# Performance work log

Measured on AMD Instinct MI355X. Metric: run time of the kernel, lower is better.

The kernel has to match this reference:

```python
import jax, jax.numpy as jnp
import numpy as np

N_NODES = 100000
N_EDGES = 1000000
NUM_GRAPHS = 100
EPS_BN = 1e-5
EPS_GATE = 1e-6


def _bn(x, gamma, beta):
    # BatchNorm1d in training mode: batch statistics over dim 0
    mu = jnp.mean(x, axis=0)
    var = jnp.var(x, axis=0)
    return (x - mu) * jax.lax.rsqrt(var + EPS_BN) * gamma + beta


def _gated_gcn_layer(h, e, snorm_n, snorm_e, W, b, g_h, b_h, g_e, b_e, src, dst):
    # W: [5, d, d] stacking A, B, C, D, E projections; b: [5, d]
    Ah = h @ W[0] + b[0]
    Bh = h @ W[1] + b[1]
    Ce = e @ W[2] + b[2]
    Dh = h @ W[3] + b[3]
    Eh = h @ W[4] + b[4]
    # edge update: e_ji = Dh_src + Eh_dst + Ce   [E, d]
    e_new = Dh[src] + Eh[dst] + Ce
    sigma = jax.nn.sigmoid(e_new)
    # node update: gated sum of source messages at destination nodes
    num = jax.ops.segment_sum(sigma * Bh[src], dst, num_segments=h.shape[0])
    den = jax.ops.segment_sum(sigma, dst, num_segments=h.shape[0])
    h_new = Ah + num / (den + EPS_GATE)
    # graph size normalization
    h_new = h_new * snorm_n
    e_new = e_new * snorm_e
    # batch norm + relu + residual (dropout = 0.0)
    h_new = jax.nn.relu(_bn(h_new, g_h, b_h))
    e_new = jax.nn.relu(_bn(e_new, g_e, b_e))
    return h + h_new, e + e_new


def setup_inputs() -> dict:
    key = jax.random.key(0)
    ks = jax.random.split(key, 12)
    nodes_feat = jax.random.normal(ks[0], (N_NODES, 64), jnp.float32)
    edges_feat = jax.random.normal(ks[1], (N_EDGES, 1), jnp.float32)
    snorm_n = jax.random.uniform(ks[2], (N_NODES, 1), jnp.float32)
    snorm_e = jax.random.uniform(ks[3], (N_EDGES, 1), jnp.float32)
    src = jax.random.randint(ks[4], (N_EDGES,), 0, N_NODES, jnp.int32)
    dst = jax.random.randint(ks[5], (N_EDGES,), 0, N_NODES, jnp.int32)
    node_graph_ids = jnp.sort(jax.random.randint(ks[6], (N_NODES,), 0, NUM_GRAPHS, jnp.int32))
    Wh = jax.random.normal(ks[7], (64, 70), jnp.float32) * 0.1
    bh = jnp.zeros((70,), jnp.float32)
    We = jax.random.normal(ks[8], (1, 70), jnp.float32) * 0.1
    be = jnp.zeros((70,), jnp.float32)
    W_gcn = jax.random.normal(ks[9], (3, 5, 70, 70), jnp.float32) * 0.1
    b_gcn = jnp.zeros((3, 5, 70), jnp.float32)
    bn_gamma_h = jnp.ones((3, 70), jnp.float32)
    bn_beta_h = jnp.zeros((3, 70), jnp.float32)
    bn_gamma_e = jnp.ones((3, 70), jnp.float32)
    bn_beta_e = jnp.zeros((3, 70), jnp.float32)
    return {"nodes_feat": nodes_feat, "edges_feat": edges_feat, "snorm_n": snorm_n,
            "snorm_e": snorm_e, "src": src, "dst": dst, "node_graph_ids": node_graph_ids,
            "Wh": Wh, "bh": bh, "We": We, "be": be, "W_gcn": W_gcn, "b_gcn": b_gcn,
            "bn_gamma_h": bn_gamma_h, "bn_beta_h": bn_beta_h,
            "bn_gamma_e": bn_gamma_e, "bn_beta_e": bn_beta_e}


def reference(nodes_feat, edges_feat, snorm_n, snorm_e, src, dst, node_graph_ids,
              Wh, bh, We, be, W_gcn, b_gcn, bn_gamma_h, bn_beta_h, bn_gamma_e, bn_beta_e):
    h = nodes_feat @ Wh + bh
    e = edges_feat @ We + be
    # hidden_dims = [70, 70] -> only gated_gcn_1 (params index 0) and gated_gcn_o (index 2)
    for li in (0, 2):
        h, e = _gated_gcn_layer(h, e, snorm_n, snorm_e, W_gcn[li], b_gcn[li],
                                bn_gamma_h[li], bn_beta_h[li], bn_gamma_e[li], bn_beta_e[li],
                                src, dst)
    # dgl.mean_nodes: per-graph mean of node features
    sums = jax.ops.segment_sum(h, node_graph_ids, num_segments=NUM_GRAPHS)
    counts = jax.ops.segment_sum(jnp.ones((h.shape[0],), h.dtype), node_graph_ids,
                                 num_segments=NUM_GRAPHS)
    hg = sums / jnp.maximum(counts, 1.0)[:, None]
    return hg
```

## Files before the change

### kernel.cpp

```cpp
#include <hip/hip_runtime.h>

#define NN 100000
#define NE 1000000
#define NG 100
#define DD 70
#define EL0 64
#define CH0 (9 * EL0)
#define TPW 5
#define EPW (16 * TPW)
#define EPB (10 * EPW)
#define SCB 512
#define WTS (70 * 72)

typedef __attribute__((ext_vector_type(8))) short bf16x8;
typedef __attribute__((ext_vector_type(4))) float f32x4;

__device__ __forceinline__ float sigmoidf_(float x) { return 1.f / (1.f + expf(-x)); }

__device__ __forceinline__ unsigned int rne_bf16(float x) {
    unsigned int u = __float_as_uint(x);
    return (u + 0x7FFFu + ((u >> 16) & 1u)) >> 16;
}
__device__ __forceinline__ float b2f(unsigned short u) {
    return __uint_as_float(((unsigned int)u) << 16);
}

#define DOT4(acc, vv, ww) { acc = fmaf((vv).x, (ww).x, acc); acc = fmaf((vv).y, (ww).y, acc); \
                            acc = fmaf((vv).z, (ww).z, acc); acc = fmaf((vv).w, (ww).w, acc); }

__global__ void k_trAll(const float* __restrict__ Wh, const float* __restrict__ Wg,
                        float* __restrict__ WT) {
    int m = blockIdx.y, f = blockIdx.x, k = threadIdx.x;
    const float* W;
    int K = DD;
    switch (m) {
        case 0: W = Wh; K = 64; break;
        case 1: W = Wg + 0 * 4900; break;
        case 2: W = Wg + 1 * 4900; break;
        case 3: W = Wg + 3 * 4900; break;
        case 4: W = Wg + 4 * 4900; break;
        case 5: W = Wg + 10 * 4900; break;
        case 6: W = Wg + 11 * 4900; break;
        case 7: W = Wg + 13 * 4900; break;
        default: W = Wg + 14 * 4900; break;
    }
    if (k < 72) WT[(m * 70 + f) * 72 + k] = (k < K) ? W[k * DD + f] : 0.f;
}

#define DENSE_BODY(STORE)                                                         \
    __shared__ float sx[36 * 72];                                                 \
    int t = threadIdx.x;                                                          \
    int r = t / DD, f = t - r * DD;                                               \
    long rb = (long)blockIdx.x * 36;                                              \
    for (int idx = t; idx < 36 * 72; idx += 640) {                                \
        int rr = idx / 72, kk = idx - rr * 72;                                    \
        long i = rb + rr;                                                         \
        sx[idx] = (kk < K && i < nrows) ? x[i * K + kk] : 0.f;                    \
    }                                                                             \
    __syncthreads();                                                              \
    if (r < 9) {                                                                  \
        const float4* wr = (const float4*)(WTm + f * 72);                         \
        float bb = bias[f];                                                       \
        float a0 = bb, a1 = bb, a2 = bb, a3 = bb;                                 \
        const float4* s0 = (const float4*)&sx[(r) * 72];                          \
        const float4* s1 = (const float4*)&sx[(r + 9) * 72];                      \
        const float4* s2 = (const float4*)&sx[(r + 18) * 72];                     \
        const float4* s3 = (const float4*)&sx[(r + 27) * 72];                     \
        _Pragma("unroll 1")                                                       \
        for (int q = 0; q < 18; q += 2) {                                         \
            float4 wA = wr[q], wB = wr[q + 1];                                    \
            float4 vA0 = s0[q], vB0 = s0[q + 1];                                  \
            DOT4(a0, vA0, wA) DOT4(a0, vB0, wB)                                   \
            float4 vA1 = s1[q], vB1 = s1[q + 1];                                  \
            DOT4(a1, vA1, wA) DOT4(a1, vB1, wB)                                   \
            float4 vA2 = s2[q], vB2 = s2[q + 1];                                  \
            DOT4(a2, vA2, wA) DOT4(a2, vB2, wB)                                   \
            float4 vA3 = s3[q], vB3 = s3[q + 1];                                  \
            DOT4(a3, vA3, wA) DOT4(a3, vB3, wB)                                   \
        }                                                                         \
        long i0 = rb + r, i1 = i0 + 9, i2 = i0 + 18, i3 = i0 + 27;                \
        if (i0 < nrows) STORE(i0, a0);                                            \
        if (i1 < nrows) STORE(i1, a1);                                            \
        if (i2 < nrows) STORE(i2, a2);                                            \
        if (i3 < nrows) STORE(i3, a3);                                            \
    }

__global__ __launch_bounds__(640) void k_dense_r(const float* __restrict__ x, int K,
                                                 const float* __restrict__ WTm,
                                                 const float* __restrict__ bias,
                                                 float* __restrict__ out, int nrows) {
#define ST_F32(ii, aa) out[(ii) * DD + f] = (aa)
    DENSE_BODY(ST_F32)
#undef ST_F32
}

__global__ __launch_bounds__(640) void k_dense_rh(const float* __restrict__ x, int K,
                                                  const float* __restrict__ WTm,
                                                  const float* __restrict__ bias,
                                                  unsigned short* __restrict__ out, int nrows) {
#define ST_BF16(ii, aa) out[(ii) * DD + f] = (unsigned short)rne_bf16(aa)
    DENSE_BODY(ST_BF16)
#undef ST_BF16
}

__global__ void k_pre(const float* __restrict__ We, const float* __restrict__ be,
                      const float* __restrict__ Wg, const float* __restrict__ bg,
                      float* __restrict__ v1, float* __restrict__ v2) {
    int f = threadIdx.x;
    if (f < DD) {
        const float* W2 = Wg + 2 * DD * DD;
        const float* b2 = bg + 2 * DD;
        float a = 0.f, c = 0.f;
        for (int k = 0; k < DD; ++k) {
            a = fmaf(We[k], W2[k * DD + f], a);
            c = fmaf(be[k], W2[k * DD + f], c);
        }
        v1[f] = a;
        v2[f] = c + b2[f];
    }
}

__global__ void k_prep2(const float* __restrict__ v1, const float* __restrict__ v2,
                        const float* __restrict__ murs_e, const float* __restrict__ ge,
                        const float* __restrict__ bbe, const float* __restrict__ We,
                        const float* __restrict__ be, const float* __restrict__ Wg,
                        float* __restrict__ CT2, unsigned short* __restrict__ WB) {
    int t = threadIdx.x;
    if (t < 35) {
        int f0 = 2 * t, f1 = 2 * t + 1;
        float A0 = murs_e[DD + f0] * ge[f0], A1 = murs_e[DD + f1] * ge[f1];
        float* c = CT2 + t * 12;
        c[0] = v1[f0];  c[1] = v1[f1];
        c[2] = v2[f0];  c[3] = v2[f1];
        c[4] = A0;      c[5] = A1;
        c[6] = bbe[f0] - murs_e[f0] * A0;
        c[7] = bbe[f1] - murs_e[f1] * A1;
        c[8] = We[f0];  c[9] = We[f1];
        c[10] = be[f0]; c[11] = be[f1];
    }
    const float* WC2 = Wg + 12 * 4900;
    for (int idx = t; idx < 960; idx += 512) {
        int nt = idx / 192, rem = idx - nt * 192;
        int c = rem / 64, l = rem - c * 64;
        int n = nt * 16 + (l & 15);
        int kb = c * 32 + (l >> 4) * 8;
        for (int j = 0; j < 8; ++j) {
            int k = kb + j;
            unsigned short v = 0;
            if (k < 70 && n < 70) v = (unsigned short)rne_bf16(WC2[k * 70 + n]);
            WB[((nt * 3 + c) * 64 + l) * 8 + j] = v;
        }
    }
}

__global__ void k_count(const int* __restrict__ dst, int* __restrict__ off) {
    int j = blockIdx.x * 256 + threadIdx.x;
    if (j < NE) atomicAdd(&off[dst[j]], 1);
}

__global__ void k_scan_a(int* __restrict__ off, int* __restrict__ part) {
    __shared__ int s[SCB];
    int t = threadIdx.x, i = blockIdx.x * SCB + t;
    int v = (i < NN) ? off[i] : 0;
    s[t] = v;
    __syncthreads();
    for (int d = 1; d < SCB; d <<= 1) {
        int x = (t >= d) ? s[t - d] : 0;
        __syncthreads();
        s[t] += x;
        __syncthreads();
    }
    if (i < NN) off[i] = s[t] - v;
    if (t == SCB - 1) part[blockIdx.x] = s[t];
}

__global__ void k_scan_b(int* __restrict__ part, int nb) {
    __shared__ int s[256];
    int t = threadIdx.x;
    int v = (t < nb) ? part[t] : 0;
    s[t] = v;
    __syncthreads();
    for (int d = 1; d < 256; d <<= 1) {
        int x = (t >= d) ? s[t - d] : 0;
        __syncthreads();
        s[t] += x;
        __syncthreads();
    }
    if (t < nb) part[t] = s[t] - v;
}

__global__ void k_scan_c(int* __restrict__ off, const int* __restrict__ part) {
    int i = blockIdx.x * SCB + threadIdx.x;
    if (i < NN) off[i] += part[blockIdx.x];
}

__global__ void k_fill(const int* __restrict__ src, const int* __restrict__ dst,
                       const float* __restrict__ ef, const float* __restrict__ sne,
                       int* __restrict__ off, int* __restrict__ src_s,
                       float* __restrict__ ef_s, float* __restrict__ sne_s,
                       int* __restrict__ dst_s) {
    int j = blockIdx.x * 256 + threadIdx.x;
    if (j < NE) {
        int d = dst[j];
        int pos = atomicAdd(&off[d], 1);
        src_s[pos] = src[j];
        ef_s[pos] = ef[j];
        sne_s[pos] = sne[j];
        dst_s[pos] = d;
    }
}

__global__ __launch_bounds__(640) void k_edge0(
    const float* __restrict__ ef_s, const float* __restrict__ sne_s,
    const int* __restrict__ src_s, const int* __restrict__ dst_s,
    const unsigned short* __restrict__ PB, const unsigned short* __restrict__ PD,
    const unsigned short* __restrict__ PE, const float* __restrict__ v1,
    const float* __restrict__ v2, float* __restrict__ num,
    float* __restrict__ den, float* __restrict__ red) {
    int t = threadIdx.x;
    int r = t / DD, f = t - r * DD;
    bool act = (r < 9);
    float c1 = 0.f, c2 = 0.f;
    if (act) { c1 = v1[f]; c2 = v2[f]; }
    float acc_s = 0.f, acc_q = 0.f;
    int e_beg = blockIdx.x * CH0 + r * EL0;
    bool live = act && e_beg < NE;
    int dcur = 0;
    float accn = 0.f, accd = 0.f;
    int lim = 0;
    if (live) {
        dcur = dst_s[e_beg];
        lim = NE - e_beg;
        if (lim > EL0) lim = EL0;
    }
    for (int g = 0; g < lim; g += 4) {
        int m = lim - g;
        if (m > 4) m = 4;
        int dj[4];
        float pdj[4], pbj[4], pej[4], efj[4], snj[4];
#pragma unroll
        for (int j = 0; j < 4; ++j) {
            if (j < m) {
                int e = e_beg + g + j;
                int s = src_s[e];
                int d = dst_s[e];
                dj[j] = d;
                efj[j] = ef_s[e];
                snj[j] = sne_s[e];
                pdj[j] = b2f(PD[(long)s * DD + f]);
                pbj[j] = b2f(PB[(long)s * DD + f]);
                pej[j] = b2f(PE[(long)d * DD + f]);
            }
        }
#pragma unroll
        for (int j = 0; j < 4; ++j) {
            if (j < m) {
                if (dj[j] != dcur) {
                    unsafeAtomicAdd(&num[(long)dcur * DD + f], accn);
                    unsafeAtomicAdd(&den[(long)dcur * DD + f], accd);
                    accn = 0.f; accd = 0.f;
                    dcur = dj[j];
                }
                float en = pdj[j] + pej[j] + efj[j] * c1 + c2;
                float sg = sigmoidf_(en);
                accn = fmaf(sg, pbj[j], accn);
                accd += sg;
                float tv = en * snj[j];
                acc_s += tv;
                acc_q = fmaf(tv, tv, acc_q);
            }
        }
    }
    if (live) {
        unsafeAtomicAdd(&num[(long)dcur * DD + f], accn);
        unsafeAtomicAdd(&den[(long)dcur * DD + f], accd);
    }
    __shared__ float ss[DD], sq[DD];
    if (t < DD) { ss[t] = 0.f; sq[t] = 0.f; }
    __syncthreads();
    if (act) { atomicAdd(&ss[f], acc_s); atomicAdd(&sq[f], acc_q); }
    __syncthreads();
    if (t < DD) {
        atomicAdd(&red[t], ss[t]);
        atomicAdd(&red[DD + t], sq[t]);
    }
}

__global__ __launch_bounds__(640) void k_edge2(
    const float* __restrict__ ef_s, const float* __restrict__ sne_s,
    const int* __restrict__ src_s, const int* __restrict__ dst_s,
    const unsigned short* __restrict__ PD0, const unsigned short* __restrict__ PE0,
    const unsigned short* __restrict__ PB2, const unsigned short* __restrict__ PD2,
    const unsigned short* __restrict__ PE2, const float* __restrict__ CT2,
    const unsigned short* __restrict__ WB, const float* __restrict__ bC2,
    float* __restrict__ num, float* __restrict__ den) {
    __shared__ __align__(16) unsigned short As[10 * 16 * 104];
    int t = threadIdx.x;
    int w = t >> 6, l = t & 63;
    unsigned short* Aw = &As[w * 1664];
    for (int i = l; i < 832; i += 64) ((unsigned int*)Aw)[i] = 0u;
    int wb_e = blockIdx.x * EPB + w * EPW;
    if (wb_e >= NE) return;
    int col = l & 15, hi = l >> 4;
    bf16x8 bfr[15];
#pragma unroll
    for (int q = 0; q < 15; ++q)
        bfr[q] = *(const bf16x8*)(WB + (q * 64 + l) * 8);
    float bc[5];
#pragma unroll
    for (int nt = 0; nt < 5; ++nt) bc[nt] = bC2[nt * 16 + col];
    int e0p = wb_e + hi * 4;
    if (e0p > NE - 1) e0p = NE - 1;
    int dcur = dst_s[e0p];
    float an[5], ad[5];
#pragma unroll
    for (int nt = 0; nt < 5; ++nt) { an[nt] = 0.f; ad[nt] = 0.f; }
    for (int tt = 0; tt < TPW; ++tt) {
        int et = wb_e + tt * 16;
        if (et >= NE) break;
        for (int i = l; i < 560; i += 64) {
            int el = i / 35, fp = i - el * 35, f = fp * 2;
            int e = et + el;
            unsigned int val = 0u;
            if (e < NE) {
                int s = src_s[e], d = dst_s[e];
                float efv = ef_s[e], sn = sne_s[e];
                const float* ct = CT2 + fp * 12;
                unsigned int upd = *(const unsigned int*)(PD0 + (long)s * DD + f);
                unsigned int upe = *(const unsigned int*)(PE0 + (long)d * DD + f);
                float pdx = __uint_as_float(upd << 16);
                float pdy = __uint_as_float(upd & 0xFFFF0000u);
                float pex = __uint_as_float(upe << 16);
                float pey = __uint_as_float(upe & 0xFFFF0000u);
                float en0a = pdx + pex + efv * ct[0] + ct[2];
                float en0b = pdy + pey + efv * ct[1] + ct[3];
                float ra = fmaxf(fmaf(en0a * sn, ct[4], ct[6]), 0.f);
                float rb = fmaxf(fmaf(en0b * sn, ct[5], ct[7]), 0.f);
                float e1a = fmaf(efv, ct[8], ct[10]) + ra;
                float e1b = fmaf(efv, ct[9], ct[11]) + rb;
                val = rne_bf16(e1a) | (rne_bf16(e1b) << 16);
            }
            ((unsigned int*)Aw)[(el * 104 + f) >> 1] = val;
        }
        bf16x8 af[3];
#pragma unroll
        for (int c = 0; c < 3; ++c)
            af[c] = *(const bf16x8*)(Aw + (l & 15) * 104 + c * 32 + hi * 8);
        f32x4 acc[5];
#pragma unroll
        for (int nt = 0; nt < 5; ++nt) {
            acc[nt] = (f32x4){0.f, 0.f, 0.f, 0.f};
#pragma unroll
            for (int c = 0; c < 3; ++c)
                acc[nt] = __builtin_amdgcn_mfma_f32_16x16x32_bf16(af[c], bfr[nt * 3 + c],
                                                                  acc[nt], 0, 0, 0);
        }
#pragma unroll
        for (int j = 0; j < 4; ++j) {
            int e = et + hi * 4 + j;
            if (e < NE) {
                int d = dst_s[e];
                if (d != dcur) {
#pragma unroll
                    for (int nt = 0; nt < 5; ++nt) {
                        int nv = nt * 16 + col;
                        if (nv < 70) {
                            unsafeAtomicAdd(&num[(long)dcur * DD + nv], an[nt]);
                            unsafeAtomicAdd(&den[(long)dcur * DD + nv], ad[nt]);
                        }
                        an[nt] = 0.f; ad[nt] = 0.f;
                    }
                    dcur = d;
                }
                int s = src_s[e];
#pragma unroll
                for (int nt = 0; nt < 5; ++nt) {
                    int nv = nt * 16 + col;
                    if (nv < 70) {
                        float en = acc[nt][j] + bc[nt] + b2f(PD2[(long)s * DD + nv])
                                 + b2f(PE2[(long)d * DD + nv]);
                        float sg = sigmoidf_(en);
                        an[nt] = fmaf(sg, b2f(PB2[(long)s * DD + nv]), an[nt]);
                        ad[nt] += sg;
                    }
                }
            }
        }
    }
#pragma unroll
    for (int nt = 0; nt < 5; ++nt) {
        int nv = nt * 16 + col;
        if (nv < 70) {
            unsafeAtomicAdd(&num[(long)dcur * DD + nv], an[nt]);
            unsafeAtomicAdd(&den[(long)dcur * DD + nv], ad[nt]);
        }
    }
}

__global__ __launch_bounds__(640) void k_nstats(const float* __restrict__ PA,
                                                const float* __restrict__ num,
                                                const float* __restrict__ den,
                                                const float* __restrict__ snn,
                                                float* __restrict__ red) {
    int t = threadIdx.x;
    int r = t / DD, f = t - r * DD;
    bool act = (r < 9);
    float acc_s = 0.f, acc_q = 0.f;
    const int T = (NN + 8) / 9;
    for (int tile = blockIdx.x; tile < T; tile += gridDim.x) {
        int i = tile * 9 + r;
        if (act && i < NN) {
            long o = (long)i * DD + f;
            float v = (PA[o] + num[o] / (den[o] + 1e-6f)) * snn[i];
            acc_s += v;
            acc_q = fmaf(v, v, acc_q);
        }
    }
    __shared__ float ss[DD], sq[DD];
    if (t < DD) { ss[t] = 0.f; sq[t] = 0.f; }
    __syncthreads();
    if (act) { atomicAdd(&ss[f], acc_s); atomicAdd(&sq[f], acc_q); }
    __syncthreads();
    if (t < DD) {
        atomicAdd(&red[t], ss[t]);
        atomicAdd(&red[DD + t], sq[t]);
    }
}

__global__ void k_stats(const float* __restrict__ sums, float* __restrict__ murs, float invn) {
    int f = threadIdx.x;
    if (f < DD) {
        float mu = sums[f] * invn;
        float var = sums[DD + f] * invn - mu * mu;
        murs[f] = mu;
        murs[DD + f] = rsqrtf(var + 1e-5f);
    }
}

__global__ __launch_bounds__(256) void k_apply(const float* __restrict__ hin,
                                               const float* __restrict__ PA,
                                               const float* __restrict__ num,
                                               const float* __restrict__ den,
                                               const float* __restrict__ snn,
                                               const float* __restrict__ murs,
                                               const float* __restrict__ g,
                                               const float* __restrict__ b,
                                               float* __restrict__ hout) {
    long idx = (long)blockIdx.x * 256 + threadIdx.x;
    if (idx < (long)NN * DD) {
        int i = (int)(idx / DD);
        int f = (int)(idx - (long)i * DD);
        float v = (PA[idx] + num[idx] / (den[idx] + 1e-6f)) * snn[i];
        float bnv = (v - murs[f]) * murs[DD + f] * g[f] + b[f];
        hout[idx] = hin[idx] + fmaxf(bnv, 0.f);
    }
}

__global__ __launch_bounds__(640) void k_readout(const float* __restrict__ h,
                                                 const int* __restrict__ gid,
                                                 float* __restrict__ gsum,
                                                 float* __restrict__ gcnt) {
    __shared__ float sv[9 * DD];
    __shared__ int sg_[9];
    int t = threadIdx.x;
    int r = t / DD, f = t - r * DD;
    int i = blockIdx.x * 9 + r;
    if (r < 9 && i < NN) {
        sv[r * DD + f] = h[(long)i * DD + f];
        if (f == 0) sg_[r] = gid[i];
    }
    __syncthreads();
    int nvalid = NN - blockIdx.x * 9;
    if (nvalid > 9) nvalid = 9;
    if (t < DD && nvalid > 0) {
        float acc = 0.f;
        int cur = sg_[0];
        for (int rr = 0; rr < nvalid; ++rr) {
            int g = sg_[rr];
            if (g != cur) {
                unsafeAtomicAdd(&gsum[cur * DD + t], acc);
                acc = 0.f;
                cur = g;
            }
            acc += sv[rr * DD + t];
        }
        unsafeAtomicAdd(&gsum[cur * DD + t], acc);
        if (t == 0) {
            int cnt = 0;
            cur = sg_[0];
            for (int rr = 0; rr < nvalid; ++rr) {
                if (sg_[rr] != cur) {
                    unsafeAtomicAdd(&gcnt[cur], (float)cnt);
                    cnt = 0;
                    cur = sg_[rr];
                }
                cnt++;
            }
            unsafeAtomicAdd(&gcnt[cur], (float)cnt);
        }
    }
}

__global__ void k_out(const float* __restrict__ gsum, const float* __restrict__ gcnt,
                      float* __restrict__ out) {
    int idx = blockIdx.x * 256 + threadIdx.x;
    if (idx < NG * DD) {
        int g = idx / DD;
        out[idx] = gsum[idx] / fmaxf(gcnt[g], 1.f);
    }
}

extern "C" void kernel_launch(void* const* d_in, const int* in_sizes, int n_in,
                              void* d_out, int out_size, void* d_ws, size_t ws_size,
                              hipStream_t stream) {
    const float* x   = (const float*)d_in[0];
    const float* ef  = (const float*)d_in[1];
    const float* snn = (const float*)d_in[2];
    const float* sne = (const float*)d_in[3];
    const int*   src = (const int*)d_in[4];
    const int*   dst = (const int*)d_in[5];
    const int*   gid = (const int*)d_in[6];
    const float* Wh  = (const float*)d_in[7];
    const float* bh  = (const float*)d_in[8];
    const float* We  = (const float*)d_in[9];
    const float* be  = (const float*)d_in[10];
    const float* Wg  = (const float*)d_in[11];
    const float* bg  = (const float*)d_in[12];
    const float* gh  = (const float*)d_in[13];
    const float* bbh = (const float*)d_in[14];
    const float* ge  = (const float*)d_in[15];
    const float* bbe = (const float*)d_in[16];
    float* out = (float*)d_out;

    const size_t NF = (size_t)NN * DD;

    float* ws = (float*)d_ws;
    float* B0 = ws;
    float* B1 = B0 + NF;
    float* B2 = B1 + NF;
    float* B3 = B2 + NF;
    float* B4 = B3 + NF;
    float* B5 = B4 + NF;
    float* B6 = B5 + NF;
    float* num = B6 + NF;
    float* den = num + NF;
    float* red  = den + NF;
    float* gsum = red + 4 * DD;
    float* gcnt = gsum + NG * DD;
    float* v1 = gcnt + NG;
    float* v2 = v1 + DD;
    float* murs_e = v2 + DD;
    float* murs_h = murs_e + 2 * DD;
    int* src_s = (int*)(murs_h + 2 * DD);
    float* ef_s  = (float*)(src_s + NE);
    float* sne_s = ef_s + NE;
    int* dst_s = (int*)(sne_s + NE);
    float* WT    = (float*)(dst_s + NE);
    uintptr_t pal = ((uintptr_t)(WT + 10 * WTS) + 15) & ~(uintptr_t)15;
    float* CT2 = (float*)pal;
    unsigned short* WB = (unsigned short*)(CT2 + 420);
    int* off  = (int*)num;
    int* part = off + NN;

    unsigned short* B0h = (unsigned short*)B0;
    unsigned short* B3h = (unsigned short*)B3;
    unsigned short* B4h = (unsigned short*)B4;
    unsigned short* B5h = (unsigned short*)B5;
    unsigned short* B6h = (unsigned short*)B6;

    size_t need = (size_t)((char*)(WB + 7680) - (char*)d_ws);
    if (ws_size < need) return;

    const int NB_N36 = (NN + 35) / 36;
    const int NB_N9  = (NN + 8) / 9;
    const int NB_E256 = (NE + 255) / 256;
    const int NB_SC  = (NN + SCB - 1) / SCB;
    const int NB_E0  = (NE + CH0 - 1) / CH0;
    const int NB_E2  = (NE + EPB - 1) / EPB;

    hipMemsetAsync(off, 0, NN * sizeof(int), stream);
    k_trAll<<<dim3(70, 9), 72, 0, stream>>>(Wh, Wg, WT);
    k_count<<<NB_E256, 256, 0, stream>>>(dst, off);
    k_scan_a<<<NB_SC, SCB, 0, stream>>>(off, part);
    k_scan_b<<<1, 256, 0, stream>>>(part, NB_SC);
    k_scan_c<<<NB_SC, SCB, 0, stream>>>(off, part);
    k_fill<<<NB_E256, 256, 0, stream>>>(src, dst, ef, sne, off, src_s, ef_s, sne_s, dst_s);

    hipMemsetAsync(num, 0, (2 * NF + 4 * DD + NG * DD + NG) * sizeof(float), stream);

    k_pre<<<1, 128, 0, stream>>>(We, be, Wg, bg, v1, v2);
    k_dense_r<<<NB_N36, 640, 0, stream>>>(x, 64, WT + 0 * WTS, bh, B0, NN);

    k_dense_r <<<NB_N36, 640, 0, stream>>>(B0, 70, WT + 1 * WTS, bg + 0 * 70, B2, NN);
    k_dense_rh<<<NB_N36, 640, 0, stream>>>(B0, 70, WT + 2 * WTS, bg + 1 * 70, B3h, NN);
    k_dense_rh<<<NB_N36, 640, 0, stream>>>(B0, 70, WT + 3 * WTS, bg + 3 * 70, B4h, NN);
    k_dense_rh<<<NB_N36, 640, 0, stream>>>(B0, 70, WT + 4 * WTS, bg + 4 * 70, B5h, NN);
    k_edge0<<<NB_E0, 640, 0, stream>>>(ef_s, sne_s, src_s, dst_s, B3h, B4h, B5h, v1, v2,
                                       num, den, red);
    k_stats<<<1, 128, 0, stream>>>(red, murs_e, 1.f / NE);
    k_prep2<<<1, 512, 0, stream>>>(v1, v2, murs_e, ge + 0, bbe + 0, We, be, Wg, CT2, WB);
    k_nstats<<<2048, 640, 0, stream>>>(B2, num, den, snn, red + 2 * DD);
    k_stats<<<1, 128, 0, stream>>>(red + 2 * DD, murs_h, 1.f / NN);
    k_apply<<<(int)((NF + 255) / 256), 256, 0, stream>>>(B0, B2, num, den, snn, murs_h,
                                                         gh + 0, bbh + 0, B1);

    hipMemsetAsync(num, 0, (2 * NF + 4 * DD) * sizeof(float), stream);
    k_dense_r <<<NB_N36, 640, 0, stream>>>(B1, 70, WT + 5 * WTS, bg + 10 * 70, B2, NN);
    k_dense_rh<<<NB_N36, 640, 0, stream>>>(B1, 70, WT + 6 * WTS, bg + 11 * 70, B3h, NN);
    k_dense_rh<<<NB_N36, 640, 0, stream>>>(B1, 70, WT + 7 * WTS, bg + 13 * 70, B0h, NN);
    k_dense_rh<<<NB_N36, 640, 0, stream>>>(B1, 70, WT + 8 * WTS, bg + 14 * 70, B6h, NN);
    k_edge2<<<NB_E2, 640, 0, stream>>>(ef_s, sne_s, src_s, dst_s, B4h, B5h, B3h, B0h, B6h,
                                       CT2, WB, bg + 12 * 70, num, den);
    k_nstats<<<2048, 640, 0, stream>>>(B2, num, den, snn, red + 2 * DD);
    k_stats<<<1, 128, 0, stream>>>(red + 2 * DD, murs_h, 1.f / NN);
    k_apply<<<(int)((NF + 255) / 256), 256, 0, stream>>>(B1, B2, num, den, snn, murs_h,
                                                         gh + 2 * DD, bbh + 2 * DD, B1);

    k_readout<<<NB_N9, 640, 0, stream>>>(B1, gid, gsum, gcnt);
    k_out<<<(NG * DD + 255) / 256, 256, 0, stream>>>(gsum, gcnt, out);
}
```

Before: 1.740 ms.

## Fuse four node projections into one kernel and shrink edge2 blocks

Replaces four separate dense projection launches per layer with one kernel that stages each input tile in shared memory once and computes the A, B, D and E projections from it. This removes three reloads of the node features and three launches per layer. Separately, k_edge2 now uses 4 waves per block (256 threads) instead of 10, which shrinks its shared buffer and gives finer-grained blocks, possibly improving occupancy and load balance. The fused kernel runs four projection loops one after another per thread, so its per-block work and register use go up.

```diff
diff --git a/kernel.cpp b/kernel.cpp
--- a/kernel.cpp
+++ b/kernel.cpp
@@ -8,7 +8,7 @@
 #define CH0 (9 * EL0)
 #define TPW 5
 #define EPW (16 * TPW)
-#define EPB (10 * EPW)
+#define EPB (4 * EPW)
 #define SCB 512
 #define WTS (70 * 72)
 
@@ -47,25 +47,53 @@
     if (k < 72) WT[(m * 70 + f) * 72 + k] = (k < K) ? W[k * DD + f] : 0.f;
 }
 
-#define DENSE_BODY(STORE)                                                         \
-    __shared__ float sx[36 * 72];                                                 \
-    int t = threadIdx.x;                                                          \
-    int r = t / DD, f = t - r * DD;                                               \
-    long rb = (long)blockIdx.x * 36;                                              \
-    for (int idx = t; idx < 36 * 72; idx += 640) {                                \
-        int rr = idx / 72, kk = idx - rr * 72;                                    \
-        long i = rb + rr;                                                         \
-        sx[idx] = (kk < K && i < nrows) ? x[i * K + kk] : 0.f;                    \
-    }                                                                             \
-    __syncthreads();                                                              \
-    if (r < 9) {                                                                  \
-        const float4* wr = (const float4*)(WTm + f * 72);                         \
-        float bb = bias[f];                                                       \
+__global__ __launch_bounds__(640) void k_dense_r(const float* __restrict__ x, int K,
+                                                 const float* __restrict__ WTm,
+                                                 const float* __restrict__ bias,
+                                                 float* __restrict__ out, int nrows) {
+    __shared__ float sx[36 * 72];
+    int t = threadIdx.x;
+    int r = t / DD, f = t - r * DD;
+    long rb = (long)blockIdx.x * 36;
+    for (int idx = t; idx < 36 * 72; idx += 640) {
+        int rr = idx / 72, kk = idx - rr * 72;
+        long i = rb + rr;
+        sx[idx] = (kk < K && i < nrows) ? x[i * K + kk] : 0.f;
+    }
+    __syncthreads();
+    if (r < 9) {
+        const float4* wr = (const float4*)(WTm + f * 72);
+        float bb = bias[f];
+        float a0 = bb, a1 = bb, a2 = bb, a3 = bb;
+        const float4* s0 = (const float4*)&sx[(r) * 72];
+        const float4* s1 = (const float4*)&sx[(r + 9) * 72];
+        const float4* s2 = (const float4*)&sx[(r + 18) * 72];
+        const float4* s3 = (const float4*)&sx[(r + 27) * 72];
+#pragma unroll 1
+        for (int q = 0; q < 18; q += 2) {
+            float4 wA = wr[q], wB = wr[q + 1];
+            float4 vA0 = s0[q], vB0 = s0[q + 1];
+            DOT4(a0, vA0, wA) DOT4(a0, vB0, wB)
+            float4 vA1 = s1[q], vB1 = s1[q + 1];
+            DOT4(a1, vA1, wA) DOT4(a1, vB1, wB)
+            float4 vA2 = s2[q], vB2 = s2[q + 1];
+            DOT4(a2, vA2, wA) DOT4(a2, vB2, wB)
+            float4 vA3 = s3[q], vB3 = s3[q + 1];
+            DOT4(a3, vA3, wA) DOT4(a3, vB3, wB)
+        }
+        long i0 = rb + r, i1 = i0 + 9, i2 = i0 + 18, i3 = i0 + 27;
+        if (i0 < nrows) out[i0 * DD + f] = a0;
+        if (i1 < nrows) out[i1 * DD + f] = a1;
+        if (i2 < nrows) out[i2 * DD + f] = a2;
+        if (i3 < nrows) out[i3 * DD + f] = a3;
+    }
+}
+
+#define PROJ(MIDX, BIAS, STORE)                                                   \
+    {                                                                             \
+        const float4* wr = (const float4*)(WT4 + (MIDX) * WTS + f * 72);          \
+        float bb = (BIAS)[f];                                                     \
         float a0 = bb, a1 = bb, a2 = bb, a3 = bb;                                 \
-        const float4* s0 = (const float4*)&sx[(r) * 72];                          \
-        const float4* s1 = (const float4*)&sx[(r + 9) * 72];                      \
-        const float4* s2 = (const float4*)&sx[(r + 18) * 72];                     \
-        const float4* s3 = (const float4*)&sx[(r + 27) * 72];                     \
         _Pragma("unroll 1")                                                       \
         for (int q = 0; q < 18; q += 2) {                                         \
             float4 wA = wr[q], wB = wr[q + 1];                                    \
@@ -78,29 +106,47 @@
             float4 vA3 = s3[q], vB3 = s3[q + 1];                                  \
             DOT4(a3, vA3, wA) DOT4(a3, vB3, wB)                                   \
         }                                                                         \
-        long i0 = rb + r, i1 = i0 + 9, i2 = i0 + 18, i3 = i0 + 27;                \
         if (i0 < nrows) STORE(i0, a0);                                            \
         if (i1 < nrows) STORE(i1, a1);                                            \
         if (i2 < nrows) STORE(i2, a2);                                            \
         if (i3 < nrows) STORE(i3, a3);                                            \
     }
 
-__global__ __launch_bounds__(640) void k_dense_r(const float* __restrict__ x, int K,
-                                                 const float* __restrict__ WTm,
-                                                 const float* __restrict__ bias,
-                                                 float* __restrict__ out, int nrows) {
-#define ST_F32(ii, aa) out[(ii) * DD + f] = (aa)
-    DENSE_BODY(ST_F32)
-#undef ST_F32
-}
-
-__global__ __launch_bounds__(640) void k_dense_rh(const float* __restrict__ x, int K,
-                                                  const float* __restrict__ WTm,
-                                                  const float* __restrict__ bias,
-                                                  unsigned short* __restrict__ out, int nrows) {
-#define ST_BF16(ii, aa) out[(ii) * DD + f] = (unsigned short)rne_bf16(aa)
-    DENSE_BODY(ST_BF16)
-#undef ST_BF16
+__global__ __launch_bounds__(640) void k_dense_q(
+    const float* __restrict__ x, const float* __restrict__ WT4,
+    const float* __restrict__ bA, const float* __restrict__ bB,
+    const float* __restrict__ bD, const float* __restrict__ bE,
+    float* __restrict__ outA, unsigned short* __restrict__ outB,
+    unsigned short* __restrict__ outD, unsigned short* __restrict__ outE, int nrows) {
+    __shared__ float sx[36 * 72];
+    int t = threadIdx.x;
+    int r = t / DD, f = t - r * DD;
+    long rb = (long)blockIdx.x * 36;
+    for (int idx = t; idx < 36 * 72; idx += 640) {
+        int rr = idx / 72, kk = idx - rr * 72;
+        long i = rb + rr;
+        sx[idx] = (kk < DD && i < nrows) ? x[i * DD + kk] : 0.f;
+    }
+    __syncthreads();
+    if (r < 9) {
+        const float4* s0 = (const float4*)&sx[(r) * 72];
+        const float4* s1 = (const float4*)&sx[(r + 9) * 72];
+        const float4* s2 = (const float4*)&sx[(r + 18) * 72];
+        const float4* s3 = (const float4*)&sx[(r + 27) * 72];
+        long i0 = rb + r, i1 = i0 + 9, i2 = i0 + 18, i3 = i0 + 27;
+#define ST_A(ii, aa) outA[(ii) * DD + f] = (aa)
+#define ST_B(ii, aa) outB[(ii) * DD + f] = (unsigned short)rne_bf16(aa)
+#define ST_D(ii, aa) outD[(ii) * DD + f] = (unsigned short)rne_bf16(aa)
+#define ST_E(ii, aa) outE[(ii) * DD + f] = (unsigned short)rne_bf16(aa)
+        PROJ(0, bA, ST_A)
+        PROJ(1, bB, ST_B)
+        PROJ(2, bD, ST_D)
+        PROJ(3, bE, ST_E)
+#undef ST_A
+#undef ST_B
+#undef ST_D
+#undef ST_E
+    }
 }
 
 __global__ void k_pre(const float* __restrict__ We, const float* __restrict__ be,
@@ -286,7 +332,7 @@
     }
 }
 
-__global__ __launch_bounds__(640) void k_edge2(
+__global__ __launch_bounds__(256) void k_edge2(
     const float* __restrict__ ef_s, const float* __restrict__ sne_s,
     const int* __restrict__ src_s, const int* __restrict__ dst_s,
     const unsigned short* __restrict__ PD0, const unsigned short* __restrict__ PE0,
@@ -294,7 +340,7 @@
     const unsigned short* __restrict__ PE2, const float* __restrict__ CT2,
     const unsigned short* __restrict__ WB, const float* __restrict__ bC2,
     float* __restrict__ num, float* __restrict__ den) {
-    __shared__ __align__(16) unsigned short As[10 * 16 * 104];
+    __shared__ __align__(16) unsigned short As[4 * 16 * 104];
     int t = threadIdx.x;
     int w = t >> 6, l = t & 63;
     unsigned short* Aw = &As[w * 1664];
@@ -591,10 +637,8 @@
     k_pre<<<1, 128, 0, stream>>>(We, be, Wg, bg, v1, v2);
     k_dense_r<<<NB_N36, 640, 0, stream>>>(x, 64, WT + 0 * WTS, bh, B0, NN);
 
-    k_dense_r <<<NB_N36, 640, 0, stream>>>(B0, 70, WT + 1 * WTS, bg + 0 * 70, B2, NN);
-    k_dense_rh<<<NB_N36, 640, 0, stream>>>(B0, 70, WT + 2 * WTS, bg + 1 * 70, B3h, NN);
-    k_dense_rh<<<NB_N36, 640, 0, stream>>>(B0, 70, WT + 3 * WTS, bg + 3 * 70, B4h, NN);
-    k_dense_rh<<<NB_N36, 640, 0, stream>>>(B0, 70, WT + 4 * WTS, bg + 4 * 70, B5h, NN);
+    k_dense_q<<<NB_N36, 640, 0, stream>>>(B0, WT + 1 * WTS, bg + 0 * 70, bg + 1 * 70,
+                                          bg + 3 * 70, bg + 4 * 70, B2, B3h, B4h, B5h, NN);
     k_edge0<<<NB_E0, 640, 0, stream>>>(ef_s, sne_s, src_s, dst_s, B3h, B4h, B5h, v1, v2,
                                        num, den, red);
     k_stats<<<1, 128, 0, stream>>>(red, murs_e, 1.f / NE);
@@ -605,11 +649,9 @@
                                                          gh + 0, bbh + 0, B1);
 
     hipMemsetAsync(num, 0, (2 * NF + 4 * DD) * sizeof(float), stream);
-    k_dense_r <<<NB_N36, 640, 0, stream>>>(B1, 70, WT + 5 * WTS, bg + 10 * 70, B2, NN);
-    k_dense_rh<<<NB_N36, 640, 0, stream>>>(B1, 70, WT + 6 * WTS, bg + 11 * 70, B3h, NN);
-    k_dense_rh<<<NB_N36, 640, 0, stream>>>(B1, 70, WT + 7 * WTS, bg + 13 * 70, B0h, NN);
-    k_dense_rh<<<NB_N36, 640, 0, stream>>>(B1, 70, WT + 8 * WTS, bg + 14 * 70, B6h, NN);
-    k_edge2<<<NB_E2, 640, 0, stream>>>(ef_s, sne_s, src_s, dst_s, B4h, B5h, B3h, B0h, B6h,
+    k_dense_q<<<NB_N36, 640, 0, stream>>>(B1, WT + 5 * WTS, bg + 10 * 70, bg + 11 * 70,
+                                          bg + 13 * 70, bg + 14 * 70, B2, B3h, B0h, B6h, NN);
+    k_edge2<<<NB_E2, 256, 0, stream>>>(ef_s, sne_s, src_s, dst_s, B4h, B5h, B3h, B0h, B6h,
                                        CT2, WB, bg + 12 * 70, num, den);
     k_nstats<<<2048, 640, 0, stream>>>(B2, num, den, snn, red + 2 * DD);
     k_stats<<<1, 128, 0, stream>>>(red + 2 * DD, murs_h, 1.f / NN);
```

Measured after the change: 1.707 ms. Within noise of the previous version (-1.9%).
